# Optimization experiments

Measured on AMD Instinct MI355X. Metric: run time of the kernel, lower is better.

The kernel has to match this reference:

```python
import jax, jax.numpy as jnp
import numpy as np

N_DYADIC = 0  # dyadic refinement order 'n' from SigLoss_MMD.__init__


def _sig_gram(X, Y, n):
    """Gram matrix of signature kernels k(x_i, y_j) via the first-order
    finite-difference PDE scheme used by sig_kernels_f/fb_mmd:
        K[i+1,j+1] = K[i+1,j] + K[i,j+1] + K[i,j]*(<dx_i, dy_j> - 1)
    with dyadically refined increments dx = (x_{t+1}-x_t)/2^n repeated 2^n times.
    X: (A, M, D), Y: (B, N, D) -> returns (A, B) = K[:, :, -1, -1].
    The row recurrence is a cumulative sum, so each PDE row is one cumsum
    (fully vectorized over all (A,B) pairs); lax.scan runs over rows.
    """
    f = 2 ** n
    incX = jnp.repeat((X[:, 1:] - X[:, :-1]) / f, f, axis=1)  # (A, MM, D)
    incY = jnp.repeat((Y[:, 1:] - Y[:, :-1]) / f, f, axis=1)  # (B, NN, D)
    Mmat = jnp.einsum('aid,bjd->abij', incX, incY)            # (A, B, MM, NN)
    A, B, MM, NN = Mmat.shape
    ones_col = jnp.ones((A, B, 1), Mmat.dtype)
    row0 = jnp.ones((A, B, NN + 1), Mmat.dtype)               # K[0, :] = 1

    def step(prev_row, Mrow):  # prev_row: (A,B,NN+1), Mrow: (A,B,NN)
        # K[i+1,j+1] - K[i+1,j] = K[i,j+1] + K[i,j]*(M[i,j]-1)  -> cumsum
        inc = prev_row[..., 1:] + prev_row[..., :-1] * (Mrow - 1.0)
        new_row = jnp.concatenate([ones_col, 1.0 + jnp.cumsum(inc, axis=-1)], axis=-1)
        return new_row, None

    last_row, _ = jax.lax.scan(step, row0, jnp.moveaxis(Mmat, 2, 0))
    return last_row[..., -1]  # (A, B)


def setup_inputs() -> dict:
    key = jax.random.key(0)
    kx, ky = jax.random.split(key)
    A, M, D = 64, 128, 128
    SCALE = 0.025  # keeps increment inner products small so the PDE stays bounded
    X = SCALE * jax.random.normal(kx, (A, M, D), dtype=jnp.float32)
    Y = SCALE * jax.random.normal(ky, (A, M, D), dtype=jnp.float32)
    return {"X": X, "Y": Y}


def reference(X, Y):
    K_XX = _sig_gram(X, X, N_DYADIC)
    K_YY = _sig_gram(Y, Y, N_DYADIC)
    K_XY = _sig_gram(X, Y, N_DYADIC)
    mmd_squared = jnp.mean(K_XX) + jnp.mean(K_YY) - 2.0 * jnp.mean(K_XY)
    return mmd_squared
```

## Files before the change

### kernel.cpp

```cpp
#include <hip/hip_runtime.h>
#include <hip/hip_bf16.h>

#define MM 127
#define CHUNK_U16 4096
#define MAT_U16   16384
#define ARR_U16   1048576
#define QS_STRIDE 136
#define QS_DWORDS (64 * QS_STRIDE)

typedef __attribute__((ext_vector_type(8))) short short8;
typedef __attribute__((ext_vector_type(4))) float floatx4;

__device__ __forceinline__ unsigned short f2bf_rne(float x) {
  unsigned int u = __float_as_uint(x);
  u += 0x7FFFu + ((u >> 16) & 1u);
  return (unsigned short)(u >> 16);
}

__device__ __forceinline__ void gload_lds16(const void* g, void* l) {
  __builtin_amdgcn_global_load_lds(
      (const __attribute__((address_space(1))) unsigned int*)g,
      (__attribute__((address_space(3))) unsigned int*)l, 16, 0, 0);
}

__device__ __forceinline__ float wave_shr1(float x) {
  return __int_as_float(__builtin_amdgcn_update_dpp(
      0, __float_as_int(x), 0x138, 0xf, 0xf, true));
}

__global__ __launch_bounds__(256) void prep_kernel(
    const float* __restrict__ X, const float* __restrict__ Y,
    unsigned short* __restrict__ base, float* __restrict__ acc)
{
  if (blockIdx.x == 0 && threadIdx.x == 0) acc[0] = 0.f;
  const int bid = blockIdx.x;
  const int c = bid & 3;
  const int m = (bid >> 2) & 63;
  const int isY = bid >> 8;
  const float* src = (isY ? Y : X) + m * 128 * 128;
  unsigned short* dst = base + isY * ARR_U16 + m * MAT_U16 + c * CHUNK_U16;

  for (int s = threadIdx.x; s < 512; s += 256) {
    const int r = s >> 2;
    const int g = (s & 3) ^ (r & 3);
    uint4 hv = make_uint4(0, 0, 0, 0);
    if (r < MM) {
      const float* p = src + r * 128 + c * 32 + g * 8;
      float4 u0 = *reinterpret_cast<const float4*>(p);
      float4 u1 = *reinterpret_cast<const float4*>(p + 4);
      float4 v0 = *reinterpret_cast<const float4*>(p + 128);
      float4 v1 = *reinterpret_cast<const float4*>(p + 132);
      float d[8] = {v0.x - u0.x, v0.y - u0.y, v0.z - u0.z, v0.w - u0.w,
                    v1.x - u1.x, v1.y - u1.y, v1.z - u1.z, v1.w - u1.w};
      unsigned int hw[4];
#pragma unroll
      for (int e = 0; e < 4; ++e) {
        float2 rr; rr.x = d[2 * e]; rr.y = d[2 * e + 1];
        __hip_bfloat162 hp = __float22bfloat162_rn(rr);
        unsigned int hu; __builtin_memcpy(&hu, &hp, 4);
        hw[e] = hu;
      }
      hv = make_uint4(hw[0], hw[1], hw[2], hw[3]);
    }
    *reinterpret_cast<uint4*>(dst + s * 8) = hv;
  }
}

__global__ __launch_bounds__(256, 4) void sig_pair_kernel(
    const unsigned short* __restrict__ base, float* __restrict__ acc)
{
  __shared__ unsigned int smw[QS_DWORDS];
  unsigned short* const sm = reinterpret_cast<unsigned short*>(smw);
  const int tid = threadIdx.x;
  const int bid = blockIdx.x;

  float w;
  int a, b, srcA, srcB;
  if (bid < 4160) {
    int p = bid;
    srcA = 0;
    if (p >= 2080) { p -= 2080; srcA = 1; }
    srcB = srcA;
    int ia = (int)((sqrtf(8.0f * (float)p + 1.0f) - 1.0f) * 0.5f);
    while ((ia + 1) * (ia + 2) / 2 <= p) ia++;
    while (ia * (ia + 1) / 2 > p) ia--;
    int ib = p - ia * (ia + 1) / 2;
    a = ia; b = ib;
    w = (a == b ? 1.0f : 2.0f) / 4096.0f;
  } else {
    int p = bid - 4160;
    a = p >> 6; b = p & 63;
    srcA = 0; srcB = 1;
    w = -2.0f / 4096.0f;
  }
  const unsigned short* Am = base + srcA * ARR_U16 + a * MAT_U16;
  const unsigned short* Bm = base + srcB * ARR_U16 + b * MAT_U16;

  const int wid = tid >> 6, lane = tid & 63;
  const int row0 = (wid >> 1) * 64, col0 = (wid & 1) * 64;
  const int lrow = lane & 15, quad = lane >> 4;

  const unsigned short* gp = ((wid < 2) ? Am : Bm) + (wid & 1) * 2048 + lane * 8;
  const unsigned int dq = wid * 2048;

  floatx4 acc4[4][4];
#pragma unroll
  for (int tr = 0; tr < 4; ++tr)
#pragma unroll
    for (int tc = 0; tc < 4; ++tc) acc4[tr][tc] = (floatx4){0.f, 0.f, 0.f, 0.f};

#pragma unroll
  for (int s = 0; s < 4; ++s)
    gload_lds16(gp + s * 512, &sm[dq + s * 512]);

  for (int c = 0; c < 4; ++c) {
    __syncthreads();
    if (c < 3) {
      const unsigned short* g = gp + (c + 1) * CHUNK_U16;
      const unsigned int db_ = ((c + 1) & 1) * 8192 + dq;
#pragma unroll
      for (int s = 0; s < 4; ++s)
        gload_lds16(g + s * 512, &sm[db_ + s * 512]);
    }
    const unsigned int bb = (c & 1) * 8192;
    short8 bh[4];
#pragma unroll
    for (int tc = 0; tc < 4; ++tc) {
      int r = col0 + tc * 16 + lrow;
      int off = r * 32 + ((quad ^ (r & 3)) * 8);
      bh[tc] = *reinterpret_cast<const short8*>(&sm[bb + 4096 + off]);
    }
#pragma unroll
    for (int tr = 0; tr < 4; ++tr) {
      int r = row0 + tr * 16 + lrow;
      int off = r * 32 + ((quad ^ (r & 3)) * 8);
      short8 ah = *reinterpret_cast<const short8*>(&sm[bb + off]);
#pragma unroll
      for (int tc = 0; tc < 4; ++tc)
        acc4[tr][tc] = __builtin_amdgcn_mfma_f32_16x16x32_bf16(ah, bh[tc], acc4[tr][tc], 0, 0, 0);
    }
  }
  __syncthreads();

  for (int i = tid; i < QS_DWORDS; i += 256) smw[i] = 0u;
  __syncthreads();

#pragma unroll
  for (int tr = 0; tr < 4; ++tr) {
#pragma unroll
    for (int tc = 0; tc < 4; ++tc) {
      int jm = col0 + tc * 16 + lrow;
#pragma unroll
      for (int e = 0; e < 4; ++e) {
        int im = row0 + tr * 16 + quad * 4 + e;
        if (im < MM && jm < MM) {
          int lt = (jm + 1) >> 1;
          int phys = im + jm + 5 - 4 * (lt >> 1) - 4 * (lt & 1);
          int half = (jm & 1) ? 0 : 1;
          sm[(lt * QS_STRIDE + phys) * 2 + half] = f2bf_rne(acc4[tr][tc][e]);
        }
      }
    }
  }
  __syncthreads();

  if (wid == (bid & 3)) {
    const int l = lane;
    const int shift = 4 * (l >> 1) + 4 * (l & 1) - 4;
    const unsigned int lbase = l * QS_STRIDE;

    auto loadg = [&](int g) -> uint4 {
      int pb = 4 * g - shift;
      pb = pb < 0 ? 132 : (pb > 128 ? 128 : pb);
      return *reinterpret_cast<const uint4*>(&smw[lbase + pb]);
    };

    float curE = 1.f, curO = 1.f;
    float npE = (l == 0) ? 0.f : 1.f, npO = 1.f;
    uint4 P0 = loadg(0), P1 = loadg(1);

    for (int g = 0; g < 63; ++g) {
      const uint4 cur = P0;
      P0 = P1;
      if (g < 62) P1 = loadg(g + 2);
      unsigned int uu[4] = {cur.x, cur.y, cur.z, cur.w};
#pragma unroll
      for (int e = 0; e < 4; ++e) {
        unsigned int u = uu[e];
        float mE = __uint_as_float(u << 16) - 1.0f;
        float mO = __uint_as_float(u & 0xFFFF0000u) - 1.0f;
        float ncE = wave_shr1(curO);
        float ncO = curE;
        float vE = (curE + npE * mE) + ncE;
        float vO = (curO + npO * mO) + ncO;
        npE = ncE; npO = ncO;
        curE = vE; curO = vO;
      }
    }
    {
      unsigned int uu[2] = {P0.x, P0.y};
#pragma unroll
      for (int e = 0; e < 2; ++e) {
        unsigned int u = uu[e];
        float mE = __uint_as_float(u << 16) - 1.0f;
        float mO = __uint_as_float(u & 0xFFFF0000u) - 1.0f;
        float ncE = wave_shr1(curO);
        float ncO = curE;
        float vE = (curE + npE * mE) + ncE;
        float vO = (curO + npO * mO) + ncO;
        npE = ncE; npO = ncO;
        curE = vE; curO = vO;
      }
    }
    if (l == 63) atomicAdd(acc, w * curO);
  }
}

__global__ void finalize_kernel(const float* __restrict__ acc,
                                unsigned int* __restrict__ out) {
  float v = acc[0];
  __hip_bfloat16 bv = __float2bfloat16(v);
  unsigned short u;
  __builtin_memcpy(&u, &bv, sizeof(u));
  out[0] = ((unsigned int)u << 16) | (unsigned int)u;
}

extern "C" void kernel_launch(void* const* d_in, const int* in_sizes, int n_in,
                              void* d_out, int out_size, void* d_ws, size_t ws_size,
                              hipStream_t stream) {
  const float* X = (const float*)d_in[0];
  const float* Y = (const float*)d_in[1];
  float* acc = (float*)d_ws;
  unsigned short* base = (unsigned short*)((char*)d_ws + 1024);

  prep_kernel<<<512, 256, 0, stream>>>(X, Y, base, acc);
  sig_pair_kernel<<<8256, 256, 0, stream>>>(base, acc);
  finalize_kernel<<<1, 1, 0, stream>>>(acc, (unsigned int*)d_out);
}
```

Measured before the change: 201.6 us.

## Process two kernel pairs per block and interleave their PDE recurrences

Each block now computes the Gram tiles for two (a,b) pairs into separate LDS slots, then one wave runs both signature-PDE recurrences interleaved so the two independent dependency chains hide each other's latency. The single atomic accumulator is replaced by 64 padded bins, summed in finalize, to cut atomic contention. The bf16 packing uses paired conversion. This doubles LDS per block, lowering occupancy to 2 blocks per CU, and halves the grid, which may reduce overlap between blocks.

Result: slower. 265.1 us (+31.5%).

```diff
diff --git a/kernel.cpp b/kernel.cpp
--- a/kernel.cpp
+++ b/kernel.cpp
@@ -6,16 +6,12 @@
 #define MAT_U16   16384
 #define ARR_U16   1048576
 #define QS_STRIDE 136
-#define QS_DWORDS (64 * QS_STRIDE)
+#define SLOT_DW   (64 * QS_STRIDE)
+#define SLOT_U16  (SLOT_DW * 2)
+#define NBIN 64
 
 typedef __attribute__((ext_vector_type(8))) short short8;
 typedef __attribute__((ext_vector_type(4))) float floatx4;
-
-__device__ __forceinline__ unsigned short f2bf_rne(float x) {
-  unsigned int u = __float_as_uint(x);
-  u += 0x7FFFu + ((u >> 16) & 1u);
-  return (unsigned short)(u >> 16);
-}
 
 __device__ __forceinline__ void gload_lds16(const void* g, void* l) {
   __builtin_amdgcn_global_load_lds(
@@ -28,11 +24,31 @@
       0, __float_as_int(x), 0x138, 0xf, 0xf, true));
 }
 
+__device__ __forceinline__ void decode_pair(int p, int& a, int& b,
+                                            int& srcA, int& srcB, float& w) {
+  if (p < 4160) {
+    srcA = 0;
+    if (p >= 2080) { p -= 2080; srcA = 1; }
+    srcB = srcA;
+    int ia = (int)((sqrtf(8.0f * (float)p + 1.0f) - 1.0f) * 0.5f);
+    while ((ia + 1) * (ia + 2) / 2 <= p) ia++;
+    while (ia * (ia + 1) / 2 > p) ia--;
+    b = p - ia * (ia + 1) / 2;
+    a = ia;
+    w = (a == b ? 1.0f : 2.0f) / 4096.0f;
+  } else {
+    p -= 4160;
+    a = p >> 6; b = p & 63;
+    srcA = 0; srcB = 1;
+    w = -2.0f / 4096.0f;
+  }
+}
+
 __global__ __launch_bounds__(256) void prep_kernel(
     const float* __restrict__ X, const float* __restrict__ Y,
-    unsigned short* __restrict__ base, float* __restrict__ acc)
+    unsigned short* __restrict__ base, float* __restrict__ bins)
 {
-  if (blockIdx.x == 0 && threadIdx.x == 0) acc[0] = 0.f;
+  if (blockIdx.x == 0 && threadIdx.x < NBIN) bins[threadIdx.x * 32] = 0.f;
   const int bid = blockIdx.x;
   const int c = bid & 3;
   const int m = (bid >> 2) & 63;
@@ -66,159 +82,164 @@
   }
 }
 
-__global__ __launch_bounds__(256, 4) void sig_pair_kernel(
-    const unsigned short* __restrict__ base, float* __restrict__ acc)
+__global__ __launch_bounds__(256, 2) void sig_pair2_kernel(
+    const unsigned short* __restrict__ base, float* __restrict__ bins)
 {
-  __shared__ unsigned int smw[QS_DWORDS];
+  extern __shared__ unsigned int smw[];
   unsigned short* const sm = reinterpret_cast<unsigned short*>(smw);
   const int tid = threadIdx.x;
   const int bid = blockIdx.x;
-
-  float w;
-  int a, b, srcA, srcB;
-  if (bid < 4160) {
-    int p = bid;
-    srcA = 0;
-    if (p >= 2080) { p -= 2080; srcA = 1; }
-    srcB = srcA;
-    int ia = (int)((sqrtf(8.0f * (float)p + 1.0f) - 1.0f) * 0.5f);
-    while ((ia + 1) * (ia + 2) / 2 <= p) ia++;
-    while (ia * (ia + 1) / 2 > p) ia--;
-    int ib = p - ia * (ia + 1) / 2;
-    a = ia; b = ib;
-    w = (a == b ? 1.0f : 2.0f) / 4096.0f;
-  } else {
-    int p = bid - 4160;
-    a = p >> 6; b = p & 63;
-    srcA = 0; srcB = 1;
-    w = -2.0f / 4096.0f;
-  }
-  const unsigned short* Am = base + srcA * ARR_U16 + a * MAT_U16;
-  const unsigned short* Bm = base + srcB * ARR_U16 + b * MAT_U16;
-
   const int wid = tid >> 6, lane = tid & 63;
   const int row0 = (wid >> 1) * 64, col0 = (wid & 1) * 64;
   const int lrow = lane & 15, quad = lane >> 4;
 
-  const unsigned short* gp = ((wid < 2) ? Am : Bm) + (wid & 1) * 2048 + lane * 8;
-  const unsigned int dq = wid * 2048;
-
-  floatx4 acc4[4][4];
-#pragma unroll
-  for (int tr = 0; tr < 4; ++tr)
-#pragma unroll
-    for (int tc = 0; tc < 4; ++tc) acc4[tr][tc] = (floatx4){0.f, 0.f, 0.f, 0.f};
-
-#pragma unroll
-  for (int s = 0; s < 4; ++s)
-    gload_lds16(gp + s * 512, &sm[dq + s * 512]);
-
-  for (int c = 0; c < 4; ++c) {
+  float wpair[2];
+
+  for (int s = 0; s < 2; ++s) {
+    int a, b, sA, sB;
+    decode_pair(2 * bid + s, a, b, sA, sB, wpair[s]);
+    const unsigned short* Am = base + sA * ARR_U16 + a * MAT_U16;
+    const unsigned short* Bm = base + sB * ARR_U16 + b * MAT_U16;
+
+    const unsigned int sbase = s * SLOT_U16;
+    const unsigned short* gp = ((wid < 2) ? Am : Bm) + (wid & 1) * 2048 + lane * 8;
+    const unsigned int dq = sbase + wid * 2048;
+
+    floatx4 acc4[4][4];
+#pragma unroll
+    for (int tr = 0; tr < 4; ++tr)
+#pragma unroll
+      for (int tc = 0; tc < 4; ++tc) acc4[tr][tc] = (floatx4){0.f, 0.f, 0.f, 0.f};
+
+#pragma unroll
+    for (int q = 0; q < 4; ++q)
+      gload_lds16(gp + q * 512, &sm[dq + q * 512]);
+
+    for (int c = 0; c < 4; ++c) {
+      __syncthreads();
+      if (c < 3) {
+        const unsigned short* g = gp + (c + 1) * CHUNK_U16;
+        const unsigned int db_ = sbase + ((c + 1) & 1) * 8192 + wid * 2048;
+#pragma unroll
+        for (int q = 0; q < 4; ++q)
+          gload_lds16(g + q * 512, &sm[db_ + q * 512]);
+      }
+      const unsigned int bb = sbase + (c & 1) * 8192;
+      short8 bh[4];
+#pragma unroll
+      for (int tc = 0; tc < 4; ++tc) {
+        int r = col0 + tc * 16 + lrow;
+        int off = r * 32 + ((quad ^ (r & 3)) * 8);
+        bh[tc] = *reinterpret_cast<const short8*>(&sm[bb + 4096 + off]);
+      }
+#pragma unroll
+      for (int tr = 0; tr < 4; ++tr) {
+        int r = row0 + tr * 16 + lrow;
+        int off = r * 32 + ((quad ^ (r & 3)) * 8);
+        short8 ah = *reinterpret_cast<const short8*>(&sm[bb + off]);
+#pragma unroll
+        for (int tc = 0; tc < 4; ++tc)
+          acc4[tr][tc] = __builtin_amdgcn_mfma_f32_16x16x32_bf16(ah, bh[tc], acc4[tr][tc], 0, 0, 0);
+      }
+    }
     __syncthreads();
-    if (c < 3) {
-      const unsigned short* g = gp + (c + 1) * CHUNK_U16;
-      const unsigned int db_ = ((c + 1) & 1) * 8192 + dq;
-#pragma unroll
-      for (int s = 0; s < 4; ++s)
-        gload_lds16(g + s * 512, &sm[db_ + s * 512]);
-    }
-    const unsigned int bb = (c & 1) * 8192;
-    short8 bh[4];
-#pragma unroll
-    for (int tc = 0; tc < 4; ++tc) {
-      int r = col0 + tc * 16 + lrow;
-      int off = r * 32 + ((quad ^ (r & 3)) * 8);
-      bh[tc] = *reinterpret_cast<const short8*>(&sm[bb + 4096 + off]);
-    }
+
+    for (int i = tid; i < SLOT_DW; i += 256) smw[s * SLOT_DW + i] = 0u;
+    __syncthreads();
+
 #pragma unroll
     for (int tr = 0; tr < 4; ++tr) {
-      int r = row0 + tr * 16 + lrow;
-      int off = r * 32 + ((quad ^ (r & 3)) * 8);
-      short8 ah = *reinterpret_cast<const short8*>(&sm[bb + off]);
-#pragma unroll
-      for (int tc = 0; tc < 4; ++tc)
-        acc4[tr][tc] = __builtin_amdgcn_mfma_f32_16x16x32_bf16(ah, bh[tc], acc4[tr][tc], 0, 0, 0);
-    }
-  }
-  __syncthreads();
-
-  for (int i = tid; i < QS_DWORDS; i += 256) smw[i] = 0u;
-  __syncthreads();
-
-#pragma unroll
-  for (int tr = 0; tr < 4; ++tr) {
-#pragma unroll
-    for (int tc = 0; tc < 4; ++tc) {
-      int jm = col0 + tc * 16 + lrow;
-#pragma unroll
-      for (int e = 0; e < 4; ++e) {
-        int im = row0 + tr * 16 + quad * 4 + e;
-        if (im < MM && jm < MM) {
+#pragma unroll
+      for (int tc = 0; tc < 4; ++tc) {
+        int jm = col0 + tc * 16 + lrow;
+        if (jm < MM) {
           int lt = (jm + 1) >> 1;
-          int phys = im + jm + 5 - 4 * (lt >> 1) - 4 * (lt & 1);
-          int half = (jm & 1) ? 0 : 1;
-          sm[(lt * QS_STRIDE + phys) * 2 + half] = f2bf_rne(acc4[tr][tc][e]);
+          int halfoff = (jm & 1) ? 0 : 1;
+          int im0 = row0 + tr * 16 + quad * 4;
+          int physb = im0 + jm + 5 - 4 * (lt >> 1) - 4 * (lt & 1);
+          unsigned int ub = sbase + (lt * QS_STRIDE + physb) * 2 + halfoff;
+#pragma unroll
+          for (int ep = 0; ep < 2; ++ep) {
+            float2 rr; rr.x = acc4[tr][tc][2 * ep]; rr.y = acc4[tr][tc][2 * ep + 1];
+            __hip_bfloat162 bp = __float22bfloat162_rn(rr);
+            unsigned int u; __builtin_memcpy(&u, &bp, 4);
+            int im = im0 + 2 * ep;
+            if (im < MM)     sm[ub + 2 * (2 * ep)]     = (unsigned short)u;
+            if (im + 1 < MM) sm[ub + 2 * (2 * ep + 1)] = (unsigned short)(u >> 16);
+          }
         }
       }
     }
-  }
-  __syncthreads();
+    __syncthreads();
+  }
 
   if (wid == (bid & 3)) {
     const int l = lane;
     const int shift = 4 * (l >> 1) + 4 * (l & 1) - 4;
     const unsigned int lbase = l * QS_STRIDE;
 
-    auto loadg = [&](int g) -> uint4 {
+    auto loadg = [&](int s, int g) -> uint4 {
       int pb = 4 * g - shift;
       pb = pb < 0 ? 132 : (pb > 128 ? 128 : pb);
-      return *reinterpret_cast<const uint4*>(&smw[lbase + pb]);
+      return *reinterpret_cast<const uint4*>(&smw[s * SLOT_DW + lbase + pb]);
     };
 
-    float curE = 1.f, curO = 1.f;
-    float npE = (l == 0) ? 0.f : 1.f, npO = 1.f;
-    uint4 P0 = loadg(0), P1 = loadg(1);
+    float curE[2] = {1.f, 1.f}, curO[2] = {1.f, 1.f};
+    float npE[2], npO[2];
+    npE[0] = npE[1] = (l == 0) ? 0.f : 1.f;
+    npO[0] = npO[1] = 1.f;
+    uint4 P0[2], P1[2];
+    P0[0] = loadg(0, 0); P0[1] = loadg(1, 0);
+    P1[0] = loadg(0, 1); P1[1] = loadg(1, 1);
 
     for (int g = 0; g < 63; ++g) {
-      const uint4 cur = P0;
-      P0 = P1;
-      if (g < 62) P1 = loadg(g + 2);
-      unsigned int uu[4] = {cur.x, cur.y, cur.z, cur.w};
+      uint4 cur0 = P0[0], cur1 = P0[1];
+      P0[0] = P1[0]; P0[1] = P1[1];
+      if (g < 62) { P1[0] = loadg(0, g + 2); P1[1] = loadg(1, g + 2); }
+      unsigned int uu0[4] = {cur0.x, cur0.y, cur0.z, cur0.w};
+      unsigned int uu1[4] = {cur1.x, cur1.y, cur1.z, cur1.w};
 #pragma unroll
       for (int e = 0; e < 4; ++e) {
-        unsigned int u = uu[e];
+#pragma unroll
+        for (int s = 0; s < 2; ++s) {
+          unsigned int u = s ? uu1[e] : uu0[e];
+          float mE = __uint_as_float(u << 16) - 1.0f;
+          float mO = __uint_as_float(u & 0xFFFF0000u) - 1.0f;
+          float ncE = wave_shr1(curO[s]);
+          float ncO = curE[s];
+          float vE = (curE[s] + npE[s] * mE) + ncE;
+          float vO = (curO[s] + npO[s] * mO) + ncO;
+          npE[s] = ncE; npO[s] = ncO;
+          curE[s] = vE; curO[s] = vO;
+        }
+      }
+    }
+#pragma unroll
+    for (int e = 0; e < 2; ++e) {
+#pragma unroll
+      for (int s = 0; s < 2; ++s) {
+        unsigned int u = e ? (s ? P0[1].y : P0[0].y) : (s ? P0[1].x : P0[0].x);
         float mE = __uint_as_float(u << 16) - 1.0f;
         float mO = __uint_as_float(u & 0xFFFF0000u) - 1.0f;
-        float ncE = wave_shr1(curO);
-        float ncO = curE;
-        float vE = (curE + npE * mE) + ncE;
-        float vO = (curO + npO * mO) + ncO;
-        npE = ncE; npO = ncO;
-        curE = vE; curO = vO;
-      }
-    }
-    {
-      unsigned int uu[2] = {P0.x, P0.y};
-#pragma unroll
-      for (int e = 0; e < 2; ++e) {
-        unsigned int u = uu[e];
-        float mE = __uint_as_float(u << 16) - 1.0f;
-        float mO = __uint_as_float(u & 0xFFFF0000u) - 1.0f;
-        float ncE = wave_shr1(curO);
-        float ncO = curE;
-        float vE = (curE + npE * mE) + ncE;
-        float vO = (curO + npO * mO) + ncO;
-        npE = ncE; npO = ncO;
-        curE = vE; curO = vO;
-      }
-    }
-    if (l == 63) atomicAdd(acc, w * curO);
-  }
-}
-
-__global__ void finalize_kernel(const float* __restrict__ acc,
+        float ncE = wave_shr1(curO[s]);
+        float ncO = curE[s];
+        float vE = (curE[s] + npE[s] * mE) + ncE;
+        float vO = (curO[s] + npO[s] * mO) + ncO;
+        npE[s] = ncE; npO[s] = ncO;
+        curE[s] = vE; curO[s] = vO;
+      }
+    }
+    if (l == 63) {
+      atomicAdd(&bins[(((bid & 31) * 2 + 0)) * 32], wpair[0] * curO[0]);
+      atomicAdd(&bins[(((bid & 31) * 2 + 1)) * 32], wpair[1] * curO[1]);
+    }
+  }
+}
+
+__global__ void finalize_kernel(const float* __restrict__ bins,
                                 unsigned int* __restrict__ out) {
-  float v = acc[0];
+  float v = 0.f;
+  for (int i = 0; i < NBIN; ++i) v += bins[i * 32];
   __hip_bfloat16 bv = __float2bfloat16(v);
   unsigned short u;
   __builtin_memcpy(&u, &bv, sizeof(u));
@@ -230,10 +251,13 @@
                               hipStream_t stream) {
   const float* X = (const float*)d_in[0];
   const float* Y = (const float*)d_in[1];
-  float* acc = (float*)d_ws;
-  unsigned short* base = (unsigned short*)((char*)d_ws + 1024);
-
-  prep_kernel<<<512, 256, 0, stream>>>(X, Y, base, acc);
-  sig_pair_kernel<<<8256, 256, 0, stream>>>(base, acc);
-  finalize_kernel<<<1, 1, 0, stream>>>(acc, (unsigned int*)d_out);
-}
+  float* bins = (float*)d_ws;
+  unsigned short* base = (unsigned short*)((char*)d_ws + 16384);
+
+  hipFuncSetAttribute(reinterpret_cast<const void*>(sig_pair2_kernel),
+                      hipFuncAttributeMaxDynamicSharedMemorySize, 69632);
+
+  prep_kernel<<<512, 256, 0, stream>>>(X, Y, base, bins);
+  sig_pair2_kernel<<<4128, 256, 69632, stream>>>(base, bins);
+  finalize_kernel<<<1, 1, 0, stream>>>(bins, (unsigned int*)d_out);
+}
```
